# Optimization experiments

Hardware: AMD Instinct MI355X
Metric: run time of the kernel (lower is better)

The kernel has to match this reference:

```python
import jax, jax.numpy as jnp
import numpy as np

B, S, D, H, E, K = 2, 2048, 512, 2048, 16, 2
LN_EPS = 1e-5


def setup_inputs() -> dict:
    key = jax.random.key(0)
    ks = jax.random.split(key, 9)
    s_in = 1.0 / np.sqrt(D)
    s_hid = 1.0 / np.sqrt(H)
    return {
        "x": jax.random.normal(ks[0], (B, S, D), dtype=jnp.float32),
        "Wg": jax.random.normal(ks[1], (D, E), dtype=jnp.float32) * s_in,
        "bg": jax.random.normal(ks[2], (E,), dtype=jnp.float32) * 0.01,
        "W1": jax.random.normal(ks[3], (E, D, H), dtype=jnp.float32) * s_in,
        "b1": jax.random.normal(ks[4], (E, H), dtype=jnp.float32) * 0.01,
        "W2": jax.random.normal(ks[5], (E, H, D), dtype=jnp.float32) * s_hid,
        "b2": jax.random.normal(ks[6], (E, D), dtype=jnp.float32) * 0.01,
        "gamma": jnp.ones((D,), dtype=jnp.float32),
        "beta": jnp.zeros((D,), dtype=jnp.float32),
    }


def reference(x, Wg, bg, W1, b1, W2, b2, gamma, beta):
    # --- top-k gating (GatingFuncTopK) ---
    logits = jnp.einsum("bsd,de->bse", x, Wg) + bg            # [B,S,E]
    probs = jax.nn.softmax(logits, axis=-1)
    topk_vals, topk_idx = jax.lax.top_k(probs, K)             # [B,S,K]
    # scatter top-k probs back into a sparse [B,S,E] routing matrix
    sparse = (jax.nn.one_hot(topk_idx, E, dtype=probs.dtype)
              * topk_vals[..., None]).sum(axis=-2)            # [B,S,E]

    # --- dense all-expert FFN (stack over experts, as in the torch code) ---
    h = jax.nn.relu(jnp.einsum("bsd,edh->ebsh", x, W1)
                    + b1[:, None, None, :])                   # [E,B,S,H]
    ex = jnp.einsum("ebsh,ehd->ebsd", h, W2) + b2[:, None, None, :]  # [E,B,S,D]

    # --- weighted combine + residual + layernorm ---
    out = jnp.einsum("bse,ebsd->bsd", sparse, ex) + x
    mu = out.mean(axis=-1, keepdims=True)
    var = ((out - mu) ** 2).mean(axis=-1, keepdims=True)
    out = (out - mu) * jax.lax.rsqrt(var + LN_EPS) * gamma + beta
    return out
```

## Files before the change

kernel.cpp:

```cpp
#include <hip/hip_runtime.h>
#include <math.h>

#define NTOK 4096
#define DDIM 512
#define HDIM 2048
#define NEXP 16


#define WS_COUNTS    0u
#define WS_OFFSETS   1024u
#define WS_NTILES    1280u
#define WS_TM        1536u
#define WS_EPOS      4096u
#define WS_TOK       36864u
#define WS_WL        299008u
#define WS_XA        1048576u
#define WS_W1T       11534336u
#define WS_W2T       45088768u
#define WS_HB        78643200u
#define WS_YB        WS_W1T

typedef __attribute__((ext_vector_type(8))) short short8;
typedef __attribute__((ext_vector_type(4))) float floatx4;
typedef unsigned short ushort_t;

__device__ __forceinline__ ushort_t f2bf(float f) {
    unsigned u = __float_as_uint(f);
    u += 0x7fffu + ((u >> 16) & 1u);
    return (ushort_t)(u >> 16);
}
__device__ __forceinline__ float bf2f(ushort_t u) {
    return __uint_as_float((unsigned)u << 16);
}

__device__ __forceinline__ void gld16(const void* g, void* l) {
    __builtin_amdgcn_global_load_lds(
        (const __attribute__((address_space(1))) unsigned*)g,
        (__attribute__((address_space(3))) unsigned*)l, 16, 0, 0);
}

#define BAR_LGKM() asm volatile("s_waitcnt lgkmcnt(0)\n\ts_barrier" ::: "memory")

__global__ __launch_bounds__(256) void gating_kernel(
    const float* __restrict__ x, const float* __restrict__ Wg,
    const float* __restrict__ bg, int* __restrict__ counts,
    int* __restrict__ tok_list, float* __restrict__ w_list,
    int* __restrict__ epos)
{
    __shared__ __align__(16) float smem[4416];
    __shared__ int lcnt[16], lbase[16];
    const int tid = threadIdx.x;
    const int bid = blockIdx.x;

    float (*xs)[520] = (float(*)[520])smem;
    float (*lsm)[16][2] = (float(*)[16][2])(smem + 4160);
    const int t0 = bid * 8;
    const float* xg = x + (size_t)t0 * DDIM;
    #pragma unroll
    for (int p = 0; p < 4; ++p) {
        const int idx = p * 1024 + tid * 4;
        *(float4*)&xs[idx >> 9][idx & 511] = *(const float4*)(xg + idx);
    }
    if (tid < 16) lcnt[tid] = 0;
    __syncthreads();
    const int tl = tid >> 5, e = (tid >> 1) & 15, h = tid & 1;
    float a0 = 0.f, a1 = 0.f, a2 = 0.f, a3 = 0.f;
    #pragma unroll 8
    for (int it = 0; it < 64; ++it) {
        const int d = h * 256 + it * 4;
        const float4 xv = *(const float4*)&xs[tl][d];
        a0 = fmaf(xv.x, Wg[(d + 0) * 16 + e], a0);
        a1 = fmaf(xv.y, Wg[(d + 1) * 16 + e], a1);
        a2 = fmaf(xv.z, Wg[(d + 2) * 16 + e], a2);
        a3 = fmaf(xv.w, Wg[(d + 3) * 16 + e], a3);
    }
    lsm[tl][e][h] = (a0 + a1) + (a2 + a3);
    __syncthreads();

    int i0 = 0, i1 = -1, r0 = 0, r1 = 0;
    float w0 = 0.f, w1 = 0.f;
    const bool tokth = ((tid & 31) == 0);
    if (tokth) {
        float l[16];
        #pragma unroll
        for (int j = 0; j < NEXP; ++j) l[j] = lsm[tl][j][0] + lsm[tl][j][1] + bg[j];
        float m = -1e30f;
        #pragma unroll
        for (int j = 0; j < NEXP; ++j) m = fmaxf(m, l[j]);
        float s = 0.f;
        #pragma unroll
        for (int j = 0; j < NEXP; ++j) s += __expf(l[j] - m);
        float v0 = -1e30f;
        #pragma unroll
        for (int j = 0; j < NEXP; ++j)
            if (l[j] > v0) { v0 = l[j]; i0 = j; }
        float v1 = -1e30f;
        #pragma unroll
        for (int j = 0; j < NEXP; ++j)
            if (j != i0 && l[j] > v1) { v1 = l[j]; i1 = j; }
        w0 = __expf(v0 - m) / s;
        w1 = __expf(v1 - m) / s;
        r0 = atomicAdd(&lcnt[i0], 1);
        r1 = atomicAdd(&lcnt[i1], 1);
    }
    __syncthreads();
    if (tid < 16 && lcnt[tid] > 0)
        lbase[tid] = atomicAdd(&counts[tid * 16], lcnt[tid]);
    __syncthreads();
    if (tokth) {
        const int t = t0 + tl;
        const int p0 = lbase[i0] + r0;
        tok_list[i0 * NTOK + p0] = t;
        w_list[i0 * NTOK + p0] = w0;
        epos[t * 2 + 0] = (i0 << 16) | p0;
        const int p1 = lbase[i1] + r1;
        tok_list[i1 * NTOK + p1] = t;
        w_list[i1 * NTOK + p1] = w1;
        epos[t * 2 + 1] = (i1 << 16) | p1;
    }
}

__global__ __launch_bounds__(256) void wtrans_kernel(
    const float* __restrict__ W1, const float* __restrict__ W2,
    ushort_t* __restrict__ W1t, ushort_t* __restrict__ W2t)
{
    __shared__ __align__(16) unsigned lds32[4224];
    const int tid = threadIdx.x;
    int bid = blockIdx.x;

    const float* src; ushort_t* dst; int C, NT, CK, e, n0, ktbase;
    if (bid < 1024) {
        e = bid >> 6; const int q = bid & 63;
        src = W1; dst = W1t; C = HDIM; NT = 128; CK = 64;
        n0 = (q & 31) << 6; ktbase = (q >> 5) << 2;
    } else {
        bid -= 1024;
        e = bid >> 6; const int q = bid & 63;
        src = W2; dst = W2t; C = DDIM; NT = 32; CK = 256;
        n0 = (q & 7) << 6; ktbase = (q >> 3) << 2;
    }
    const int kq = tid >> 4, cc4 = (tid & 15) << 2;
    const int w = tid >> 6, l = tid & 63;
    const float* sp = src + (size_t)e * (DDIM * HDIM) + n0;
    ushort_t* run = dst + ((size_t)e * NT + (n0 >> 4) + w) * ((size_t)CK * 128);

    float4 v[2][4];
    #pragma unroll
    for (int p = 0; p < 4; ++p)
        v[0][p] = *(const float4*)(sp + (size_t)((ktbase + 0) * 64 + kq * 4 + p) * C + cc4);
    #pragma unroll
    for (int p = 0; p < 4; ++p)
        v[1][p] = *(const float4*)(sp + (size_t)((ktbase + 1) * 64 + kq * 4 + p) * C + cc4);

    #pragma unroll
    for (int i = 0; i < 4; ++i) {
        unsigned* lb = lds32 + (i & 1) * 2112;
        const float4* vv = v[i & 1];
        #pragma unroll
        for (int p2 = 0; p2 < 2; ++p2) {
            const float4 a = vv[2 * p2], b = vv[2 * p2 + 1];
            const int kp = kq * 2 + p2;
            lb[(cc4 + 0) * 33 + kp] = (unsigned)f2bf(a.x) | ((unsigned)f2bf(b.x) << 16);
            lb[(cc4 + 1) * 33 + kp] = (unsigned)f2bf(a.y) | ((unsigned)f2bf(b.y) << 16);
            lb[(cc4 + 2) * 33 + kp] = (unsigned)f2bf(a.z) | ((unsigned)f2bf(b.z) << 16);
            lb[(cc4 + 3) * 33 + kp] = (unsigned)f2bf(a.w) | ((unsigned)f2bf(b.w) << 16);
        }
        if (i < 2) {
            #pragma unroll
            for (int p = 0; p < 4; ++p)
                v[i & 1][p] = *(const float4*)(
                    sp + (size_t)((ktbase + i + 2) * 64 + kq * 4 + p) * C + cc4);
        }
        BAR_LGKM();
        const int kt = ktbase + i;
        ushort_t* runp = run + (size_t)kt * 1024;
        #pragma unroll
        for (int s = 0; s < 2; ++s) {
            const int kc = s * 4 + (l >> 4);
            const unsigned* rp = lb + (w * 16 + (l & 15)) * 33 + kc * 4;
            const unsigned o0 = rp[0], o1 = rp[1], o2 = rp[2], o3 = rp[3];
            *(uint4*)(runp + (size_t)s * 512 + l * 8) = make_uint4(o0, o1, o2, o3);
        }
    }
}

__global__ void scan_kernel(const int* __restrict__ counts, int* __restrict__ offsets,
                            int* __restrict__ tm, int* __restrict__ ntiles)
{
    const int lane = threadIdx.x;
    int c = (lane < NEXP) ? counts[lane * 16] : 0;
    int t = (c + 127) >> 7;
    int ic = c, it = t;
    #pragma unroll
    for (int off = 1; off < 16; off <<= 1) {
        const int pc = __shfl_up(ic, off, 64);
        const int pt = __shfl_up(it, off, 64);
        if (lane >= off) { ic += pc; it += pt; }
    }
    if (lane < NEXP) {
        offsets[lane] = ic - c;
        if (lane == NEXP - 1) { offsets[NEXP] = ic; ntiles[0] = it; }
        const int tb = it - t;
        for (int i = 0; i < t; ++i) tm[tb + i] = (lane << 16) | i;
    }
}

__global__ __launch_bounds__(256) void gather_xa(
    const float* __restrict__ x, const int* __restrict__ tok_list,
    const int* __restrict__ counts, const int* __restrict__ tm,
    const int* __restrict__ ntiles, ushort_t* __restrict__ xa)
{
    const int b = blockIdx.x;
    if (b >= ntiles[0]) return;
    const int info = tm[b];
    const int e = info >> 16, m0 = (info & 0xffff) << 7;
    const int Me = counts[e * 16];
    const int row = threadIdx.x >> 1;
    const int half = threadIdx.x & 1;
    const int kbase = blockIdx.y * 128 + half * 64;
    const int tok = tok_list[e * NTOK + min(m0 + row, Me - 1)];
    const float* src = x + (size_t)tok * DDIM + kbase;
    ushort_t* dstb = xa + (size_t)b * 65536 + (size_t)(row >> 4) * 8192 + (row & 15) * 8;
    #pragma unroll
    for (int q = 0; q < 16; ++q) {
        const int k = kbase + q * 4;
        const float4 v = *(const float4*)(src + q * 4);
        ushort4 o = make_ushort4(f2bf(v.x), f2bf(v.y), f2bf(v.z), f2bf(v.w));
        *(ushort4*)(dstb + (size_t)(k >> 3) * 128 + (k & 7)) = o;
    }
}

__global__ __launch_bounds__(256) void gemm1_mfma(
    const ushort_t* __restrict__ xa, const ushort_t* __restrict__ W1t,
    const float* __restrict__ b1, const int* __restrict__ tm,
    const int* __restrict__ ntiles, ushort_t* __restrict__ hb)
{
    const int t = blockIdx.y;
    if (t >= ntiles[0]) return;
    const int e = tm[t] >> 16;
    const int n0 = blockIdx.x << 7;
    const int tid = threadIdx.x, lane = tid & 63, w = tid >> 6;
    const int fm = lane & 15, fq = lane >> 4;
    const int wr = (w >> 1) << 6, wc = (w & 1) << 6;

    __shared__ __align__(16) ushort_t lds[16384];

    const ushort_t* gA = xa + (size_t)t * 65536 + lane * 8;
    const ushort_t* gB = W1t + ((size_t)e * 128 + (n0 >> 4)) * 8192 + lane * 8;
    const int s0 = w, s1 = w + 4;

    #define G1_STAGE(d, kc) do {                                            \
        ushort_t* lb_ = &lds[(d) * 8192];                                   \
        gld16(gA + (size_t)s0 * 8192 + (kc) * 512, lb_ + s0 * 512);         \
        gld16(gA + (size_t)s1 * 8192 + (kc) * 512, lb_ + s1 * 512);         \
        gld16(gB + (size_t)s0 * 8192 + (kc) * 512, lb_ + 4096 + s0 * 512);  \
        gld16(gB + (size_t)s1 * 8192 + (kc) * 512, lb_ + 4096 + s1 * 512);  \
    } while (0)

    G1_STAGE(0, 0);
    __syncthreads();

    floatx4 acc[4][4] = {};
    for (int kc = 0; kc < 16; ++kc) {
        const int d = kc & 1;
        if (kc < 15) G1_STAGE(d ^ 1, kc + 1);
        const ushort_t* la = &lds[d * 8192 + (wr >> 4) * 512 + lane * 8];
        const ushort_t* lbB = &lds[d * 8192 + 4096 + (wc >> 4) * 512 + lane * 8];
        short8 af[4], bf[4];
        #pragma unroll
        for (int i = 0; i < 4; ++i) af[i] = *(const short8*)(la + i * 512);
        #pragma unroll
        for (int j = 0; j < 4; ++j) bf[j] = *(const short8*)(lbB + j * 512);
        #pragma unroll
        for (int i = 0; i < 4; ++i)
            #pragma unroll
            for (int j = 0; j < 4; ++j)
                acc[i][j] = __builtin_amdgcn_mfma_f32_16x16x32_bf16(
                    af[i], bf[j], acc[i][j], 0, 0, 0);
        __syncthreads();
    }
    #undef G1_STAGE

    ushort_t* ls = lds;
    #pragma unroll
    for (int j = 0; j < 4; ++j) {
        const float bias = b1[(size_t)e * HDIM + n0 + wc + j * 16 + fm];
        #pragma unroll
        for (int i = 0; i < 4; ++i)
            #pragma unroll
            for (int r = 0; r < 4; ++r) {
                const int row = wr + i * 16 + fq * 4 + r;
                ls[row * 128 + wc + j * 16 + fm] =
                    f2bf(fmaxf(acc[i][j][r] + bias, 0.f));
            }
    }
    __syncthreads();
    ushort_t* hbase = hb + (size_t)t * 262144 + (size_t)(n0 >> 3) * 128;
    #pragma unroll
    for (int p = 0; p < 8; ++p) {
        const int unit = tid + p * 256;
        const int row = unit >> 4, c16 = unit & 15;
        *(short8*)(hbase + (size_t)(row >> 4) * 32768 + (size_t)c16 * 128
                   + (row & 15) * 8) = *(const short8*)&ls[row * 128 + c16 * 8];
    }
}

__global__ __launch_bounds__(256) void gemm2_mfma(
    const ushort_t* __restrict__ hb, const ushort_t* __restrict__ W2t,
    const float* __restrict__ b2, const float* __restrict__ w_list,
    const int* __restrict__ counts, const int* __restrict__ offsets,
    const int* __restrict__ tm, const int* __restrict__ ntiles,
    ushort_t* __restrict__ yb)
{
    const int t = blockIdx.y;
    if (t >= ntiles[0]) return;
    const int info = tm[t];
    const int e = info >> 16, m0 = (info & 0xffff) << 7;
    const int Me = counts[e * 16], aoff = offsets[e];
    const int n0 = blockIdx.x << 7;
    const int kz = blockIdx.z;
    const int tid = threadIdx.x, lane = tid & 63, w = tid >> 6;
    const int fm = lane & 15, fq = lane >> 4;
    const int wr = (w >> 1) << 6, wc = (w & 1) << 6;

    __shared__ __align__(16) ushort_t lds[16384];

    const ushort_t* gA = hb + (size_t)t * 262144 + (size_t)kz * 8192 + lane * 8;
    const ushort_t* gB = W2t + ((size_t)e * 32 + (n0 >> 4)) * 32768
                       + (size_t)kz * 8192 + lane * 8;
    const int s0 = w, s1 = w + 4;

    #define G2_STAGE(d, kc) do {                                            \
        ushort_t* lb_ = &lds[(d) * 8192];                                   \
        gld16(gA + (size_t)s0 * 32768 + (kc) * 512, lb_ + s0 * 512);        \
        gld16(gA + (size_t)s1 * 32768 + (kc) * 512, lb_ + s1 * 512);        \
        gld16(gB + (size_t)s0 * 32768 + (kc) * 512, lb_ + 4096 + s0 * 512); \
        gld16(gB + (size_t)s1 * 32768 + (kc) * 512, lb_ + 4096 + s1 * 512); \
    } while (0)

    G2_STAGE(0, 0);
    __syncthreads();

    floatx4 acc[4][4] = {};
    for (int kc = 0; kc < 16; ++kc) {
        const int d = kc & 1;
        if (kc < 15) G2_STAGE(d ^ 1, kc + 1);
        const ushort_t* la = &lds[d * 8192 + (wr >> 4) * 512 + lane * 8];
        const ushort_t* lbB = &lds[d * 8192 + 4096 + (wc >> 4) * 512 + lane * 8];
        short8 af[4], bf[4];
        #pragma unroll
        for (int i = 0; i < 4; ++i) af[i] = *(const short8*)(la + i * 512);
        #pragma unroll
        for (int j = 0; j < 4; ++j) bf[j] = *(const short8*)(lbB + j * 512);
        #pragma unroll
        for (int i = 0; i < 4; ++i)
            #pragma unroll
            for (int j = 0; j < 4; ++j)
                acc[i][j] = __builtin_amdgcn_mfma_f32_16x16x32_bf16(
                    af[i], bf[j], acc[i][j], 0, 0, 0);
        __syncthreads();
    }
    #undef G2_STAGE

    ushort_t* ls = lds;
    #pragma unroll
    for (int j = 0; j < 4; ++j) {
        const float bias = (kz == 0) ? b2[(size_t)e * DDIM + n0 + wc + j * 16 + fm] : 0.f;
        #pragma unroll
        for (int i = 0; i < 4; ++i)
            #pragma unroll
            for (int r = 0; r < 4; ++r) {
                const int row = wr + i * 16 + fq * 4 + r;
                const float gw = w_list[e * NTOK + min(m0 + row, Me - 1)];
                ls[row * 128 + wc + j * 16 + fm] = f2bf(gw * (acc[i][j][r] + bias));
            }
    }
    __syncthreads();
    ushort_t* ybase = yb + (size_t)kz * (8192 * 512) + n0;
    #pragma unroll
    for (int p = 0; p < 8; ++p) {
        const int unit = tid + p * 256;
        const int row = unit >> 4, c16 = unit & 15;
        if (m0 + row < Me)
            *(short8*)(ybase + (size_t)(aoff + m0 + row) * 512 + c16 * 8)
                = *(const short8*)&ls[row * 128 + c16 * 8];
    }
}

__global__ __launch_bounds__(256) void ln_kernel(
    const float* __restrict__ x, const ushort_t* __restrict__ yb,
    const int* __restrict__ epos, const int* __restrict__ offsets,
    const float* __restrict__ gamma, const float* __restrict__ beta,
    float* __restrict__ out)
{
    const int t = blockIdx.x * 4 + (threadIdx.x >> 6);
    const int lane = threadIdx.x & 63;
    const int d0 = lane * 8;

    const int p0 = epos[2 * t + 0];
    const int p1 = epos[2 * t + 1];
    const size_t r0 = (size_t)(offsets[p0 >> 16] + (p0 & 0xFFFF));
    const size_t r1 = (size_t)(offsets[p1 >> 16] + (p1 & 0xFFFF));

    short8 ys[8];
    #pragma unroll
    for (int kz = 0; kz < 4; ++kz) {
        ys[kz * 2 + 0] = *(const short8*)(yb + (size_t)kz * (8192 * 512) + r0 * 512 + d0);
        ys[kz * 2 + 1] = *(const short8*)(yb + (size_t)kz * (8192 * 512) + r1 * 512 + d0);
    }
    float xv[8];
    *(float4*)&xv[0] = *(const float4*)(x + (size_t)t * DDIM + d0);
    *(float4*)&xv[4] = *(const float4*)(x + (size_t)t * DDIM + d0 + 4);

    float v[8];
    float s = 0.f;
    #pragma unroll
    for (int i = 0; i < 8; ++i) {
        float a = xv[i];
        #pragma unroll
        for (int q = 0; q < 8; ++q) a += bf2f((ushort_t)ys[q][i]);
        v[i] = a;
        s += a;
    }
    #pragma unroll
    for (int o = 32; o > 0; o >>= 1) s += __shfl_xor(s, o, 64);
    const float mu = s * (1.f / DDIM);
    float q = 0.f;
    #pragma unroll
    for (int i = 0; i < 8; ++i) { const float d_ = v[i] - mu; q = fmaf(d_, d_, q); }
    #pragma unroll
    for (int o = 32; o > 0; o >>= 1) q += __shfl_xor(q, o, 64);
    const float rstd = rsqrtf(q * (1.f / DDIM) + 1e-5f);

    float g[8], bt[8], o8[8];
    *(float4*)&g[0] = *(const float4*)(gamma + d0);
    *(float4*)&g[4] = *(const float4*)(gamma + d0 + 4);
    *(float4*)&bt[0] = *(const float4*)(beta + d0);
    *(float4*)&bt[4] = *(const float4*)(beta + d0 + 4);
    #pragma unroll
    for (int i = 0; i < 8; ++i) o8[i] = (v[i] - mu) * rstd * g[i] + bt[i];
    *(float4*)(out + (size_t)t * DDIM + d0) = *(float4*)&o8[0];
    *(float4*)(out + (size_t)t * DDIM + d0 + 4) = *(float4*)&o8[4];
}

extern "C" void kernel_launch(void* const* d_in, const int* in_sizes, int n_in,
                              void* d_out, int out_size, void* d_ws, size_t ws_size,
                              hipStream_t stream) {
    const float* x     = (const float*)d_in[0];
    const float* Wg    = (const float*)d_in[1];
    const float* bg    = (const float*)d_in[2];
    const float* W1    = (const float*)d_in[3];
    const float* b1    = (const float*)d_in[4];
    const float* W2    = (const float*)d_in[5];
    const float* b2    = (const float*)d_in[6];
    const float* gamma = (const float*)d_in[7];
    const float* beta  = (const float*)d_in[8];
    float* out = (float*)d_out;

    char* ws = (char*)d_ws;
    int*      counts   = (int*)(ws + WS_COUNTS);
    int*      offsets  = (int*)(ws + WS_OFFSETS);
    int*      ntiles   = (int*)(ws + WS_NTILES);
    int*      tm       = (int*)(ws + WS_TM);
    int*      epos     = (int*)(ws + WS_EPOS);
    int*      tok_list = (int*)(ws + WS_TOK);
    float*    w_list   = (float*)(ws + WS_WL);
    ushort_t* xa       = (ushort_t*)(ws + WS_XA);
    ushort_t* W1t      = (ushort_t*)(ws + WS_W1T);
    ushort_t* W2t      = (ushort_t*)(ws + WS_W2T);
    ushort_t* hb       = (ushort_t*)(ws + WS_HB);
    ushort_t* yb       = (ushort_t*)(ws + WS_YB);

    hipMemsetAsync(counts, 0, 1024, stream);
    gating_kernel<<<512, 256, 0, stream>>>(x, Wg, bg, counts, tok_list, w_list, epos);
    wtrans_kernel<<<2048, 256, 0, stream>>>(W1, W2, W1t, W2t);
    scan_kernel<<<1, 64, 0, stream>>>(counts, offsets, tm, ntiles);
    gather_xa<<<dim3(80, 4), 256, 0, stream>>>(x, tok_list, counts, tm, ntiles, xa);
    gemm1_mfma<<<dim3(HDIM / 128, 80), 256, 0, stream>>>(
        xa, W1t, b1, tm, ntiles, hb);
    gemm2_mfma<<<dim3(DDIM / 128, 80, 4), 256, 0, stream>>>(
        hb, W2t, b2, w_list, counts, offsets, tm, ntiles, yb);
    ln_kernel<<<NTOK / 4, 256, 0, stream>>>(x, yb, epos, offsets, gamma, beta, out);
}
```

Measured before the change: 299.9 us.

## Fuse weight transposes into gating and gemm1 kernels to overlap work

Removes the standalone weight-transpose kernel. The W1 bf16 transpose now runs as extra blocks of the gating kernel, and the W2 transpose runs as extra blocks of the gemm1 kernel. The point is to overlap this memory-bound conversion with compute-light or independent work and to save a launch. The transpose tiling also changes to 32-row slices with a single LDS buffer. The W2 transpose blocks now share the device with gemm1 blocks, and the W1t-dependent gemm1 still waits on the whole fused gating launch.

```diff
diff --git a/kernel.cpp b/kernel.cpp
--- a/kernel.cpp
+++ b/kernel.cpp
@@ -39,18 +39,60 @@
         (__attribute__((address_space(3))) unsigned*)l, 16, 0, 0);
 }
 
-#define BAR_LGKM() asm volatile("s_waitcnt lgkmcnt(0)\n\ts_barrier" ::: "memory")
-
-__global__ __launch_bounds__(256) void gating_kernel(
+__device__ __forceinline__ void wtrans_tile(
+    const float* __restrict__ src, ushort_t* __restrict__ dst,
+    int C, int NT, int CK, int e, int ks, int nw, unsigned* lb, int tid)
+{
+    const int q = tid >> 4;
+    const int c0 = (tid & 15) << 2;
+    const float* sp = src + (size_t)e * (DDIM * HDIM)
+                    + (size_t)(ks * 32 + 2 * q) * C + nw * 256;
+    float4 va[4], vb[4];
+    #pragma unroll
+    for (int p = 0; p < 4; ++p) {
+        va[p] = *(const float4*)(sp + c0 + p * 64);
+        vb[p] = *(const float4*)(sp + C + c0 + p * 64);
+    }
+    #pragma unroll
+    for (int p = 0; p < 4; ++p) {
+        const int n = c0 + p * 64;
+        lb[(n + 0) * 17 + q] = (unsigned)f2bf(va[p].x) | ((unsigned)f2bf(vb[p].x) << 16);
+        lb[(n + 1) * 17 + q] = (unsigned)f2bf(va[p].y) | ((unsigned)f2bf(vb[p].y) << 16);
+        lb[(n + 2) * 17 + q] = (unsigned)f2bf(va[p].z) | ((unsigned)f2bf(vb[p].z) << 16);
+        lb[(n + 3) * 17 + q] = (unsigned)f2bf(va[p].w) | ((unsigned)f2bf(vb[p].w) << 16);
+    }
+    __syncthreads();
+    const int nt = tid >> 4, nl = tid & 15;
+    const int ntg = nw * 16 + nt;
+    ushort_t* rbase = dst + ((size_t)e * NT + ntg) * ((size_t)CK * 128) + nl * 8;
+    const unsigned* rp = lb + (nt * 16 + nl) * 17;
+    #pragma unroll
+    for (int kc = 0; kc < 4; ++kc) {
+        const unsigned o0 = rp[kc * 4 + 0], o1 = rp[kc * 4 + 1];
+        const unsigned o2 = rp[kc * 4 + 2], o3 = rp[kc * 4 + 3];
+        *(uint4*)(rbase + (size_t)(ks * 4 + kc) * 128) = make_uint4(o0, o1, o2, o3);
+    }
+}
+
+__global__ __launch_bounds__(256) void fusedA_kernel(
     const float* __restrict__ x, const float* __restrict__ Wg,
     const float* __restrict__ bg, int* __restrict__ counts,
     int* __restrict__ tok_list, float* __restrict__ w_list,
-    int* __restrict__ epos)
+    int* __restrict__ epos, const float* __restrict__ W1,
+    ushort_t* __restrict__ W1t)
 {
     __shared__ __align__(16) float smem[4416];
     __shared__ int lcnt[16], lbase[16];
     const int tid = threadIdx.x;
-    const int bid = blockIdx.x;
+    int bid = blockIdx.x;
+
+    if (bid >= 512) {
+        bid -= 512;
+        const int e = bid >> 7, r = bid & 127;
+        const int nw = r & 7, ks = r >> 3;
+        wtrans_tile(W1, W1t, HDIM, 128, 64, e, ks, nw, (unsigned*)smem, tid);
+        return;
+    }
 
     float (*xs)[520] = (float(*)[520])smem;
     float (*lsm)[16][2] = (float(*)[16][2])(smem + 4160);
@@ -117,70 +159,6 @@
         tok_list[i1 * NTOK + p1] = t;
         w_list[i1 * NTOK + p1] = w1;
         epos[t * 2 + 1] = (i1 << 16) | p1;
-    }
-}
-
-__global__ __launch_bounds__(256) void wtrans_kernel(
-    const float* __restrict__ W1, const float* __restrict__ W2,
-    ushort_t* __restrict__ W1t, ushort_t* __restrict__ W2t)
-{
-    __shared__ __align__(16) unsigned lds32[4224];
-    const int tid = threadIdx.x;
-    int bid = blockIdx.x;
-
-    const float* src; ushort_t* dst; int C, NT, CK, e, n0, ktbase;
-    if (bid < 1024) {
-        e = bid >> 6; const int q = bid & 63;
-        src = W1; dst = W1t; C = HDIM; NT = 128; CK = 64;
-        n0 = (q & 31) << 6; ktbase = (q >> 5) << 2;
-    } else {
-        bid -= 1024;
-        e = bid >> 6; const int q = bid & 63;
-        src = W2; dst = W2t; C = DDIM; NT = 32; CK = 256;
-        n0 = (q & 7) << 6; ktbase = (q >> 3) << 2;
-    }
-    const int kq = tid >> 4, cc4 = (tid & 15) << 2;
-    const int w = tid >> 6, l = tid & 63;
-    const float* sp = src + (size_t)e * (DDIM * HDIM) + n0;
-    ushort_t* run = dst + ((size_t)e * NT + (n0 >> 4) + w) * ((size_t)CK * 128);
-
-    float4 v[2][4];
-    #pragma unroll
-    for (int p = 0; p < 4; ++p)
-        v[0][p] = *(const float4*)(sp + (size_t)((ktbase + 0) * 64 + kq * 4 + p) * C + cc4);
-    #pragma unroll
-    for (int p = 0; p < 4; ++p)
-        v[1][p] = *(const float4*)(sp + (size_t)((ktbase + 1) * 64 + kq * 4 + p) * C + cc4);
-
-    #pragma unroll
-    for (int i = 0; i < 4; ++i) {
-        unsigned* lb = lds32 + (i & 1) * 2112;
-        const float4* vv = v[i & 1];
-        #pragma unroll
-        for (int p2 = 0; p2 < 2; ++p2) {
-            const float4 a = vv[2 * p2], b = vv[2 * p2 + 1];
-            const int kp = kq * 2 + p2;
-            lb[(cc4 + 0) * 33 + kp] = (unsigned)f2bf(a.x) | ((unsigned)f2bf(b.x) << 16);
-            lb[(cc4 + 1) * 33 + kp] = (unsigned)f2bf(a.y) | ((unsigned)f2bf(b.y) << 16);
-            lb[(cc4 + 2) * 33 + kp] = (unsigned)f2bf(a.z) | ((unsigned)f2bf(b.z) << 16);
-            lb[(cc4 + 3) * 33 + kp] = (unsigned)f2bf(a.w) | ((unsigned)f2bf(b.w) << 16);
-        }
-        if (i < 2) {
-            #pragma unroll
-            for (int p = 0; p < 4; ++p)
-                v[i & 1][p] = *(const float4*)(
-                    sp + (size_t)((ktbase + i + 2) * 64 + kq * 4 + p) * C + cc4);
-        }
-        BAR_LGKM();
-        const int kt = ktbase + i;
-        ushort_t* runp = run + (size_t)kt * 1024;
-        #pragma unroll
-        for (int s = 0; s < 2; ++s) {
-            const int kc = s * 4 + (l >> 4);
-            const unsigned* rp = lb + (w * 16 + (l & 15)) * 33 + kc * 4;
-            const unsigned o0 = rp[0], o1 = rp[1], o2 = rp[2], o3 = rp[3];
-            *(uint4*)(runp + (size_t)s * 512 + l * 8) = make_uint4(o0, o1, o2, o3);
-        }
     }
 }
 
@@ -230,20 +208,31 @@
     }
 }
 
-__global__ __launch_bounds__(256) void gemm1_mfma(
+__global__ __launch_bounds__(256) void fusedC_kernel(
     const ushort_t* __restrict__ xa, const ushort_t* __restrict__ W1t,
     const float* __restrict__ b1, const int* __restrict__ tm,
-    const int* __restrict__ ntiles, ushort_t* __restrict__ hb)
-{
-    const int t = blockIdx.y;
+    const int* __restrict__ ntiles, ushort_t* __restrict__ hb,
+    const float* __restrict__ W2, ushort_t* __restrict__ W2t)
+{
+    __shared__ __align__(16) ushort_t lds[16384];
+    const int tid = threadIdx.x;
+    const int bid = blockIdx.x;
+
+    if (bid >= 1280) {
+        const int wb = bid - 1280;
+        const int e = wb >> 7, r = wb & 127;
+        const int nw = r & 1, ks = r >> 1;
+        wtrans_tile(W2, W2t, DDIM, 32, 256, e, ks, nw, (unsigned*)lds, tid);
+        return;
+    }
+
+    const int t = bid >> 4;
     if (t >= ntiles[0]) return;
     const int e = tm[t] >> 16;
-    const int n0 = blockIdx.x << 7;
-    const int tid = threadIdx.x, lane = tid & 63, w = tid >> 6;
+    const int n0 = (bid & 15) << 7;
+    const int lane = tid & 63, w = tid >> 6;
     const int fm = lane & 15, fq = lane >> 4;
     const int wr = (w >> 1) << 6, wc = (w & 1) << 6;
-
-    __shared__ __align__(16) ushort_t lds[16384];
 
     const ushort_t* gA = xa + (size_t)t * 65536 + lane * 8;
     const ushort_t* gB = W1t + ((size_t)e * 128 + (n0 >> 4)) * 8192 + lane * 8;
@@ -472,12 +461,11 @@
     ushort_t* yb       = (ushort_t*)(ws + WS_YB);
 
     hipMemsetAsync(counts, 0, 1024, stream);
-    gating_kernel<<<512, 256, 0, stream>>>(x, Wg, bg, counts, tok_list, w_list, epos);
-    wtrans_kernel<<<2048, 256, 0, stream>>>(W1, W2, W1t, W2t);
+    fusedA_kernel<<<2560, 256, 0, stream>>>(x, Wg, bg, counts, tok_list, w_list,
+                                            epos, W1, W1t);
     scan_kernel<<<1, 64, 0, stream>>>(counts, offsets, tm, ntiles);
     gather_xa<<<dim3(80, 4), 256, 0, stream>>>(x, tok_list, counts, tm, ntiles, xa);
-    gemm1_mfma<<<dim3(HDIM / 128, 80), 256, 0, stream>>>(
-        xa, W1t, b1, tm, ntiles, hb);
+    fusedC_kernel<<<3328, 256, 0, stream>>>(xa, W1t, b1, tm, ntiles, hb, W2, W2t);
     gemm2_mfma<<<dim3(DDIM / 128, 80, 4), 256, 0, stream>>>(
         hb, W2t, b2, w_list, counts, offsets, tm, ntiles, yb);
     ln_kernel<<<NTOK / 4, 256, 0, stream>>>(x, yb, epos, offsets, gamma, beta, out);
```

Result: faster. 276.5 us (-7.8%).
